# Optimization experiments

Hardware: AMD Instinct MI355X
Metric: run time of the kernel (lower is better)

Reference implementation:

```python
import jax, jax.numpy as jnp
import numpy as np

NUM_HIGH = 3
CHANNELS = 3

def _gauss_kernel(channels):
    k = jnp.array([[1., 4., 6., 4., 1.],
                   [4., 16., 24., 16., 4.],
                   [6., 24., 36., 24., 6.],
                   [4., 16., 24., 16., 4.],
                   [1., 4., 6., 4., 1.]], dtype=jnp.float32) / 256.0
    # depthwise kernel layout OIHW with I=1, O=channels
    return jnp.broadcast_to(k, (channels, 1, 5, 5))

def conv_gauss(img, kernel):
    # reflect-pad by 2 on H,W then depthwise (grouped) 5x5 conv, VALID
    p = jnp.pad(img, ((0, 0), (0, 0), (2, 2), (2, 2)), mode='reflect')
    return jax.lax.conv_general_dilated(
        p, kernel, window_strides=(1, 1), padding='VALID',
        feature_group_count=img.shape[1],
        dimension_numbers=('NCHW', 'OIHW', 'NCHW'))

def downsample(x):
    return x[:, :, ::2, ::2]

def upsample(x, kernel):
    B, C, H, W = x.shape
    x_up = jnp.zeros((B, C, 2 * H, 2 * W), dtype=x.dtype).at[:, :, ::2, ::2].set(x)
    return conv_gauss(x_up, 4.0 * kernel)

def setup_inputs() -> dict:
    key = jax.random.key(0)
    img = jax.random.normal(key, (8, CHANNELS, 1024, 1024), dtype=jnp.float32)
    kernel = _gauss_kernel(CHANNELS)
    return {"img": img, "kernel": kernel}

def reference(img, kernel):
    # pyramid_decom: Laplacian pyramid (H,W divisible by 2**NUM_HIGH, so no interpolate)
    current = img
    pyr = []
    for _ in range(NUM_HIGH):
        filtered = conv_gauss(current, kernel)
        down = downsample(filtered)
        up = upsample(down, kernel)
        pyr.append(current - up)
        current = down
    pyr.append(current)
    return tuple(pyr)
```

## Files before the change

### kernel.cpp

```cpp
#include <hip/hip_runtime.h>

#define TW 64
#define TH 32
#define DR 18
#define DC 34
#define TMPP 76
#define SDP 35

__device__ __forceinline__ int refl(int t, int n) {
    if (t < 0) t = -t;
    if (t >= n) t = 2 * (n - 1) - t;
    return t;
}

__global__ __launch_bounds__(256, 8) void lap_level_kernel(
    const float* __restrict__ cur, float* __restrict__ lap,
    float* __restrict__ down, int H, int W)
{
    __shared__ float s_tmp[DR][TMPP];
    __shared__ float s_down[DR][SDP];

    const int x0 = blockIdx.x * TW, y0 = blockIdx.y * TH;
    const int img = blockIdx.z;
    const int Hh = H >> 1, Wh = W >> 1;
    const int tid = threadIdx.x;

    const float* curb = cur + (size_t)img * H * W;

    const bool border = (x0 == 0) | (y0 == 0) | (x0 + TW == W) | (y0 + TH == H);
    if (!border) {
        for (int k = tid; k < DR * 18; k += 256) {
            unsigned a = (unsigned)k / 18u;
            unsigned c4 = ((unsigned)k - a * 18u) * 4u;
            const float* p = curb + (size_t)(y0 + 2 * (int)a - 4) * W + (x0 - 4 + (int)c4);
            float4 r0 = *(const float4*)(p);
            float4 r1 = *(const float4*)(p + (size_t)W);
            float4 r2 = *(const float4*)(p + (size_t)2 * W);
            float4 r3 = *(const float4*)(p + (size_t)3 * W);
            float4 r4 = *(const float4*)(p + (size_t)4 * W);
            float4 t;
            t.x = r0.x + 4.f * r1.x + 6.f * r2.x + 4.f * r3.x + r4.x;
            t.y = r0.y + 4.f * r1.y + 6.f * r2.y + 4.f * r3.y + r4.y;
            t.z = r0.z + 4.f * r1.z + 6.f * r2.z + 4.f * r3.z + r4.z;
            t.w = r0.w + 4.f * r1.w + 6.f * r2.w + 4.f * r3.w + r4.w;
            *(float4*)&s_tmp[a][c4] = t;
        }
    } else {
        for (int k = tid; k < DR * 72; k += 256) {
            unsigned a = (unsigned)k / 72u;
            unsigned c = (unsigned)k - a * 72u;
            int gx = refl(x0 - 4 + (int)c, W);
            int r0 = y0 + 2 * (int)a - 4;
            float acc = 0.f;
            const float wv[5] = {1.f, 4.f, 6.f, 4.f, 1.f};
#pragma unroll
            for (int u = 0; u < 5; ++u)
                acc += wv[u] * curb[(size_t)refl(r0 + u, H) * W + gx];
            s_tmp[a][c] = acc;
        }
    }
    __syncthreads();

    float* downb = down + (size_t)img * Hh * Wh;
    for (int k = tid; k < DR * 17; k += 256) {
        unsigned a = (unsigned)k / 17u;
        unsigned b2 = (unsigned)k - a * 17u;
        float4 A = *(const float4*)&s_tmp[a][4 * b2];
        float4 B = *(const float4*)&s_tmp[a][4 * b2 + 4];
        float v0 = (A.x + 4.f * A.y + 6.f * A.z + 4.f * A.w + B.x) * (1.f / 256.f);
        float v1 = (A.z + 4.f * A.w + 6.f * B.x + 4.f * B.y + B.z) * (1.f / 256.f);
        s_down[a][2 * b2] = v0;
        s_down[a][2 * b2 + 1] = v1;
        if (a - 1u < 16u) {
            size_t rowoff = (size_t)((y0 >> 1) - 1 + (int)a) * Wh + ((x0 >> 1) - 1);
            if (b2 >= 1u) downb[rowoff + 2 * b2] = v0;
            if (b2 <= 15u) downb[rowoff + 2 * b2 + 1] = v1;
        }
    }
    __syncthreads();

    const int tx = tid & 15, ty = tid >> 4;
    float d0[4], d1[4], d2[4];
#pragma unroll
    for (int c = 0; c < 4; ++c) {
        d0[c] = s_down[ty + 0][2 * tx + c];
        d1[c] = s_down[ty + 1][2 * tx + c];
        d2[c] = s_down[ty + 2][2 * tx + c];
    }
    float ce[4], co[4];
#pragma unroll
    for (int c = 0; c < 4; ++c) {
        ce[c] = d0[c] + 6.f * d1[c] + d2[c];
        co[c] = 4.f * (d1[c] + d2[c]);
    }
    const int i0 = y0 + 2 * ty, j0 = x0 + 4 * tx;
    const float* cvp = curb + (size_t)i0 * W + j0;
    float4 cve = *(const float4*)(cvp);
    float4 cvo = *(const float4*)(cvp + (size_t)W);
    float4 oe, oo;
    oe.x = cve.x - (ce[0] + 6.f * ce[1] + ce[2]) * (1.f / 64.f);
    oe.y = cve.y - 4.f * (ce[1] + ce[2]) * (1.f / 64.f);
    oe.z = cve.z - (ce[1] + 6.f * ce[2] + ce[3]) * (1.f / 64.f);
    oe.w = cve.w - 4.f * (ce[2] + ce[3]) * (1.f / 64.f);
    oo.x = cvo.x - (co[0] + 6.f * co[1] + co[2]) * (1.f / 64.f);
    oo.y = cvo.y - 4.f * (co[1] + co[2]) * (1.f / 64.f);
    oo.z = cvo.z - (co[1] + 6.f * co[2] + co[3]) * (1.f / 64.f);
    oo.w = cvo.w - 4.f * (co[2] + co[3]) * (1.f / 64.f);

    float* lapb = lap + (size_t)img * H * W;
    *(float4*)(lapb + (size_t)i0 * W + j0) = oe;
    *(float4*)(lapb + (size_t)(i0 + 1) * W + j0) = oo;
}

extern "C" void kernel_launch(void* const* d_in, const int* in_sizes, int n_in,
                              void* d_out, int out_size, void* d_ws, size_t ws_size,
                              hipStream_t stream) {
    const float* img = (const float*)d_in[0];
    float* out = (float*)d_out;

    const long long BC = 8LL * 3;
    const long long n0 = BC * 1024 * 1024;
    const long long n1 = BC * 512 * 512;
    const long long n2 = BC * 256 * 256;

    float* out0 = out;
    float* out1 = out0 + n0;
    float* out2 = out1 + n1;
    float* out3 = out2 + n2;

    float* ws0 = (float*)d_ws;
    float* ws1 = ws0 + n1;

    lap_level_kernel<<<dim3(1024 / TW, 1024 / TH, (int)BC), 256, 0, stream>>>(
        img, out0, ws0, 1024, 1024);
    lap_level_kernel<<<dim3(512 / TW, 512 / TH, (int)BC), 256, 0, stream>>>(
        ws0, out1, ws1, 512, 512);
    lap_level_kernel<<<dim3(256 / TW, 256 / TH, (int)BC), 256, 0, stream>>>(
        ws1, out2, out3, 256, 256);
}
```

Before: 81.03 us.

## Fuse vertical and horizontal blur into one pass, drop intermediate smem stage

Merges the vertical 5-tap pass and the horizontal 5-tap/downsample pass into a single per-thread computation that reads two float4s per row directly from global memory. This removes the s_tmp shared buffer and one __syncthreads. The center-pixel loads are hoisted to the top of the kernel so their latency overlaps the blur work, and the Laplacian output uses nontemporal stores. In exchange, the overlapping 8-wide reads fetch more global data, roughly twice the column loads, which the cache must absorb.

```diff
diff --git a/kernel.cpp b/kernel.cpp
--- a/kernel.cpp
+++ b/kernel.cpp
@@ -4,8 +4,10 @@
 #define TH 32
 #define DR 18
 #define DC 34
-#define TMPP 76
 #define SDP 35
+#define NTASK (DR * 17)
+
+typedef float vf4 __attribute__((ext_vector_type(4)));
 
 __device__ __forceinline__ int refl(int t, int n) {
     if (t < 0) t = -t;
@@ -13,73 +15,92 @@
     return t;
 }
 
+__device__ __forceinline__ void nt_store4(float x, float y, float z, float w, float* p) {
+    vf4 v = {x, y, z, w};
+    __builtin_nontemporal_store(v, (vf4*)p);
+}
+
 __global__ __launch_bounds__(256, 8) void lap_level_kernel(
     const float* __restrict__ cur, float* __restrict__ lap,
     float* __restrict__ down, int H, int W)
 {
-    __shared__ float s_tmp[DR][TMPP];
     __shared__ float s_down[DR][SDP];
 
     const int x0 = blockIdx.x * TW, y0 = blockIdx.y * TH;
     const int img = blockIdx.z;
     const int Hh = H >> 1, Wh = W >> 1;
     const int tid = threadIdx.x;
+    const int tx = tid & 15, ty = tid >> 4;
 
     const float* curb = cur + (size_t)img * H * W;
 
+    const int i0 = y0 + 2 * ty, j0 = x0 + 4 * tx;
+    const float* cvp = curb + (size_t)i0 * W + j0;
+    const float4 cve = *(const float4*)(cvp);
+    const float4 cvo = *(const float4*)(cvp + (size_t)W);
+
+    float* downb = down + (size_t)img * Hh * Wh;
     const bool border = (x0 == 0) | (y0 == 0) | (x0 + TW == W) | (y0 + TH == H);
     if (!border) {
-        for (int k = tid; k < DR * 18; k += 256) {
-            unsigned a = (unsigned)k / 18u;
-            unsigned c4 = ((unsigned)k - a * 18u) * 4u;
-            const float* p = curb + (size_t)(y0 + 2 * (int)a - 4) * W + (x0 - 4 + (int)c4);
-            float4 r0 = *(const float4*)(p);
-            float4 r1 = *(const float4*)(p + (size_t)W);
-            float4 r2 = *(const float4*)(p + (size_t)2 * W);
-            float4 r3 = *(const float4*)(p + (size_t)3 * W);
-            float4 r4 = *(const float4*)(p + (size_t)4 * W);
-            float4 t;
-            t.x = r0.x + 4.f * r1.x + 6.f * r2.x + 4.f * r3.x + r4.x;
-            t.y = r0.y + 4.f * r1.y + 6.f * r2.y + 4.f * r3.y + r4.y;
-            t.z = r0.z + 4.f * r1.z + 6.f * r2.z + 4.f * r3.z + r4.z;
-            t.w = r0.w + 4.f * r1.w + 6.f * r2.w + 4.f * r3.w + r4.w;
-            *(float4*)&s_tmp[a][c4] = t;
+        for (int k = tid; k < NTASK; k += 256) {
+            unsigned a = (unsigned)k / 17u;
+            unsigned b2 = (unsigned)k - a * 17u;
+            const float* p = curb + (size_t)(y0 - 4 + 2 * (int)a) * W + (x0 - 4 + 4 * (int)b2);
+            float4 A0 = *(const float4*)(p);
+            float4 B0 = *(const float4*)(p + 4);
+            float4 A1 = *(const float4*)(p + (size_t)W);
+            float4 B1 = *(const float4*)(p + (size_t)W + 4);
+            float4 A2 = *(const float4*)(p + (size_t)2 * W);
+            float4 B2 = *(const float4*)(p + (size_t)2 * W + 4);
+            float4 A3 = *(const float4*)(p + (size_t)3 * W);
+            float4 B3 = *(const float4*)(p + (size_t)3 * W + 4);
+            float4 A4 = *(const float4*)(p + (size_t)4 * W);
+            float4 B4 = *(const float4*)(p + (size_t)4 * W + 4);
+            float s0 = A0.x + 4.f * A1.x + 6.f * A2.x + 4.f * A3.x + A4.x;
+            float s1 = A0.y + 4.f * A1.y + 6.f * A2.y + 4.f * A3.y + A4.y;
+            float s2 = A0.z + 4.f * A1.z + 6.f * A2.z + 4.f * A3.z + A4.z;
+            float s3 = A0.w + 4.f * A1.w + 6.f * A2.w + 4.f * A3.w + A4.w;
+            float s4 = B0.x + 4.f * B1.x + 6.f * B2.x + 4.f * B3.x + B4.x;
+            float s5 = B0.y + 4.f * B1.y + 6.f * B2.y + 4.f * B3.y + B4.y;
+            float s6 = B0.z + 4.f * B1.z + 6.f * B2.z + 4.f * B3.z + B4.z;
+            float v0 = (s0 + 4.f * s1 + 6.f * s2 + 4.f * s3 + s4) * (1.f / 256.f);
+            float v1 = (s2 + 4.f * s3 + 6.f * s4 + 4.f * s5 + s6) * (1.f / 256.f);
+            s_down[a][2 * b2] = v0;
+            s_down[a][2 * b2 + 1] = v1;
+            if (a - 1u < 16u) {
+                size_t rowoff = (size_t)((y0 >> 1) - 1 + (int)a) * Wh + ((x0 >> 1) - 1);
+                if (b2 >= 1u) downb[rowoff + 2 * b2] = v0;
+                if (b2 <= 15u) downb[rowoff + 2 * b2 + 1] = v1;
+            }
         }
     } else {
-        for (int k = tid; k < DR * 72; k += 256) {
-            unsigned a = (unsigned)k / 72u;
-            unsigned c = (unsigned)k - a * 72u;
-            int gx = refl(x0 - 4 + (int)c, W);
-            int r0 = y0 + 2 * (int)a - 4;
-            float acc = 0.f;
+        for (int k = tid; k < NTASK; k += 256) {
+            unsigned a = (unsigned)k / 17u;
+            unsigned b2 = (unsigned)k - a * 17u;
             const float wv[5] = {1.f, 4.f, 6.f, 4.f, 1.f};
+            float s[7];
 #pragma unroll
-            for (int u = 0; u < 5; ++u)
-                acc += wv[u] * curb[(size_t)refl(r0 + u, H) * W + gx];
-            s_tmp[a][c] = acc;
+            for (int c = 0; c < 7; ++c) {
+                int gx = refl(x0 - 4 + 4 * (int)b2 + c, W);
+                float acc = 0.f;
+#pragma unroll
+                for (int u = 0; u < 5; ++u)
+                    acc += wv[u] * curb[(size_t)refl(y0 - 4 + 2 * (int)a + u, H) * W + gx];
+                s[c] = acc;
+            }
+            float v0 = (s[0] + 4.f * s[1] + 6.f * s[2] + 4.f * s[3] + s[4]) * (1.f / 256.f);
+            float v1 = (s[2] + 4.f * s[3] + 6.f * s[4] + 4.f * s[5] + s[6]) * (1.f / 256.f);
+            s_down[a][2 * b2] = v0;
+            s_down[a][2 * b2 + 1] = v1;
+            if (a - 1u < 16u) {
+                size_t rowoff = (size_t)((y0 >> 1) - 1 + (int)a) * Wh + ((x0 >> 1) - 1);
+                if (b2 >= 1u) downb[rowoff + 2 * b2] = v0;
+                if (b2 <= 15u) downb[rowoff + 2 * b2 + 1] = v1;
+            }
         }
     }
     __syncthreads();
 
-    float* downb = down + (size_t)img * Hh * Wh;
-    for (int k = tid; k < DR * 17; k += 256) {
-        unsigned a = (unsigned)k / 17u;
-        unsigned b2 = (unsigned)k - a * 17u;
-        float4 A = *(const float4*)&s_tmp[a][4 * b2];
-        float4 B = *(const float4*)&s_tmp[a][4 * b2 + 4];
-        float v0 = (A.x + 4.f * A.y + 6.f * A.z + 4.f * A.w + B.x) * (1.f / 256.f);
-        float v1 = (A.z + 4.f * A.w + 6.f * B.x + 4.f * B.y + B.z) * (1.f / 256.f);
-        s_down[a][2 * b2] = v0;
-        s_down[a][2 * b2 + 1] = v1;
-        if (a - 1u < 16u) {
-            size_t rowoff = (size_t)((y0 >> 1) - 1 + (int)a) * Wh + ((x0 >> 1) - 1);
-            if (b2 >= 1u) downb[rowoff + 2 * b2] = v0;
-            if (b2 <= 15u) downb[rowoff + 2 * b2 + 1] = v1;
-        }
-    }
-    __syncthreads();
-
-    const int tx = tid & 15, ty = tid >> 4;
     float d0[4], d1[4], d2[4];
 #pragma unroll
     for (int c = 0; c < 4; ++c) {
@@ -93,23 +114,17 @@
         ce[c] = d0[c] + 6.f * d1[c] + d2[c];
         co[c] = 4.f * (d1[c] + d2[c]);
     }
-    const int i0 = y0 + 2 * ty, j0 = x0 + 4 * tx;
-    const float* cvp = curb + (size_t)i0 * W + j0;
-    float4 cve = *(const float4*)(cvp);
-    float4 cvo = *(const float4*)(cvp + (size_t)W);
-    float4 oe, oo;
-    oe.x = cve.x - (ce[0] + 6.f * ce[1] + ce[2]) * (1.f / 64.f);
-    oe.y = cve.y - 4.f * (ce[1] + ce[2]) * (1.f / 64.f);
-    oe.z = cve.z - (ce[1] + 6.f * ce[2] + ce[3]) * (1.f / 64.f);
-    oe.w = cve.w - 4.f * (ce[2] + ce[3]) * (1.f / 64.f);
-    oo.x = cvo.x - (co[0] + 6.f * co[1] + co[2]) * (1.f / 64.f);
-    oo.y = cvo.y - 4.f * (co[1] + co[2]) * (1.f / 64.f);
-    oo.z = cvo.z - (co[1] + 6.f * co[2] + co[3]) * (1.f / 64.f);
-    oo.w = cvo.w - 4.f * (co[2] + co[3]) * (1.f / 64.f);
-
     float* lapb = lap + (size_t)img * H * W;
-    *(float4*)(lapb + (size_t)i0 * W + j0) = oe;
-    *(float4*)(lapb + (size_t)(i0 + 1) * W + j0) = oo;
+    nt_store4(cve.x - (ce[0] + 6.f * ce[1] + ce[2]) * (1.f / 64.f),
+              cve.y - 4.f * (ce[1] + ce[2]) * (1.f / 64.f),
+              cve.z - (ce[1] + 6.f * ce[2] + ce[3]) * (1.f / 64.f),
+              cve.w - 4.f * (ce[2] + ce[3]) * (1.f / 64.f),
+              lapb + (size_t)i0 * W + j0);
+    nt_store4(cvo.x - (co[0] + 6.f * co[1] + co[2]) * (1.f / 64.f),
+              cvo.y - 4.f * (co[1] + co[2]) * (1.f / 64.f),
+              cvo.z - (co[1] + 6.f * co[2] + co[3]) * (1.f / 64.f),
+              cvo.w - 4.f * (co[2] + co[3]) * (1.f / 64.f),
+              lapb + (size_t)(i0 + 1) * W + j0);
 }
 
 extern "C" void kernel_launch(void* const* d_in, const int* in_sizes, int n_in,
```

New measurement: 185.2 us. 2.29x slower.

## Widen tiles to 128 columns and compute two filtered rows per thread

Applied to the files above, without the earlier changes.

Doubles the tile width to 128 columns, so each thread in the final stage produces 8 Laplacian outputs per row instead of 4, and the column halo overhead per tile shrinks. The vertical filter pass now has each thread load 7 input rows and emit two downsampled-row partial sums, reusing 3 rows between them. The separate border and interior paths are merged into one path that reflects row indices always and falls back to scalar gathers only for edge columns. Fewer blocks and more work per thread trade parallelism for reuse, and at the smaller levels the grid becomes small, with fewer blocks to spread across the CUs.

```diff
diff --git a/kernel.cpp b/kernel.cpp
--- a/kernel.cpp
+++ b/kernel.cpp
@@ -1,11 +1,11 @@
 #include <hip/hip_runtime.h>
 
-#define TW 64
+#define TW 128
 #define TH 32
 #define DR 18
-#define DC 34
-#define TMPP 76
-#define SDP 35
+#define NC4 34
+#define TMPP 140
+#define SDP 67
 
 __device__ __forceinline__ int refl(int t, int n) {
     if (t < 0) t = -t;
@@ -27,89 +27,102 @@
 
     const float* curb = cur + (size_t)img * H * W;
 
-    const bool border = (x0 == 0) | (y0 == 0) | (x0 + TW == W) | (y0 + TH == H);
-    if (!border) {
-        for (int k = tid; k < DR * 18; k += 256) {
-            unsigned a = (unsigned)k / 18u;
-            unsigned c4 = ((unsigned)k - a * 18u) * 4u;
-            const float* p = curb + (size_t)(y0 + 2 * (int)a - 4) * W + (x0 - 4 + (int)c4);
-            float4 r0 = *(const float4*)(p);
-            float4 r1 = *(const float4*)(p + (size_t)W);
-            float4 r2 = *(const float4*)(p + (size_t)2 * W);
-            float4 r3 = *(const float4*)(p + (size_t)3 * W);
-            float4 r4 = *(const float4*)(p + (size_t)4 * W);
-            float4 t;
-            t.x = r0.x + 4.f * r1.x + 6.f * r2.x + 4.f * r3.x + r4.x;
-            t.y = r0.y + 4.f * r1.y + 6.f * r2.y + 4.f * r3.y + r4.y;
-            t.z = r0.z + 4.f * r1.z + 6.f * r2.z + 4.f * r3.z + r4.z;
-            t.w = r0.w + 4.f * r1.w + 6.f * r2.w + 4.f * r3.w + r4.w;
-            *(float4*)&s_tmp[a][c4] = t;
+    for (int k = tid; k < 9 * NC4; k += 256) {
+        int e = k / NC4, c4 = k - e * NC4;
+        int colg = x0 - 4 + 4 * c4;
+        int rows[7];
+#pragma unroll
+        for (int u = 0; u < 7; ++u) rows[u] = refl(y0 - 4 + 4 * e + u, H);
+        float4 r[7];
+        if (colg >= 0 && colg + 3 < W) {
+#pragma unroll
+            for (int u = 0; u < 7; ++u)
+                r[u] = *(const float4*)(curb + (size_t)rows[u] * W + colg);
+        } else {
+            int gx[4];
+#pragma unroll
+            for (int cc = 0; cc < 4; ++cc) gx[cc] = refl(colg + cc, W);
+#pragma unroll
+            for (int u = 0; u < 7; ++u) {
+                const float* rp = curb + (size_t)rows[u] * W;
+                r[u].x = rp[gx[0]]; r[u].y = rp[gx[1]];
+                r[u].z = rp[gx[2]]; r[u].w = rp[gx[3]];
+            }
         }
-    } else {
-        for (int k = tid; k < DR * 72; k += 256) {
-            unsigned a = (unsigned)k / 72u;
-            unsigned c = (unsigned)k - a * 72u;
-            int gx = refl(x0 - 4 + (int)c, W);
-            int r0 = y0 + 2 * (int)a - 4;
-            float acc = 0.f;
-            const float wv[5] = {1.f, 4.f, 6.f, 4.f, 1.f};
-#pragma unroll
-            for (int u = 0; u < 5; ++u)
-                acc += wv[u] * curb[(size_t)refl(r0 + u, H) * W + gx];
-            s_tmp[a][c] = acc;
-        }
+        float4 t0, t1;
+        t0.x = r[0].x + 4.f * r[1].x + 6.f * r[2].x + 4.f * r[3].x + r[4].x;
+        t0.y = r[0].y + 4.f * r[1].y + 6.f * r[2].y + 4.f * r[3].y + r[4].y;
+        t0.z = r[0].z + 4.f * r[1].z + 6.f * r[2].z + 4.f * r[3].z + r[4].z;
+        t0.w = r[0].w + 4.f * r[1].w + 6.f * r[2].w + 4.f * r[3].w + r[4].w;
+        t1.x = r[2].x + 4.f * r[3].x + 6.f * r[4].x + 4.f * r[5].x + r[6].x;
+        t1.y = r[2].y + 4.f * r[3].y + 6.f * r[4].y + 4.f * r[5].y + r[6].y;
+        t1.z = r[2].z + 4.f * r[3].z + 6.f * r[4].z + 4.f * r[5].z + r[6].z;
+        t1.w = r[2].w + 4.f * r[3].w + 6.f * r[4].w + 4.f * r[5].w + r[6].w;
+        *(float4*)&s_tmp[2 * e][4 * c4] = t0;
+        *(float4*)&s_tmp[2 * e + 1][4 * c4] = t1;
     }
     __syncthreads();
 
     float* downb = down + (size_t)img * Hh * Wh;
-    for (int k = tid; k < DR * 17; k += 256) {
-        unsigned a = (unsigned)k / 17u;
-        unsigned b2 = (unsigned)k - a * 17u;
+    for (int k = tid; k < DR * 33; k += 256) {
+        int a = k / 33, b2 = k - a * 33;
         float4 A = *(const float4*)&s_tmp[a][4 * b2];
         float4 B = *(const float4*)&s_tmp[a][4 * b2 + 4];
         float v0 = (A.x + 4.f * A.y + 6.f * A.z + 4.f * A.w + B.x) * (1.f / 256.f);
         float v1 = (A.z + 4.f * A.w + 6.f * B.x + 4.f * B.y + B.z) * (1.f / 256.f);
         s_down[a][2 * b2] = v0;
         s_down[a][2 * b2 + 1] = v1;
-        if (a - 1u < 16u) {
-            size_t rowoff = (size_t)((y0 >> 1) - 1 + (int)a) * Wh + ((x0 >> 1) - 1);
-            if (b2 >= 1u) downb[rowoff + 2 * b2] = v0;
-            if (b2 <= 15u) downb[rowoff + 2 * b2 + 1] = v1;
+        if ((unsigned)(a - 1) < 16u) {
+            size_t rowoff = (size_t)((y0 >> 1) - 1 + a) * Wh + ((x0 >> 1) - 1);
+            if (b2 >= 1) downb[rowoff + 2 * b2] = v0;
+            if (b2 <= 31) downb[rowoff + 2 * b2 + 1] = v1;
         }
     }
     __syncthreads();
 
     const int tx = tid & 15, ty = tid >> 4;
-    float d0[4], d1[4], d2[4];
+    float d0[6], d1[6], d2[6];
 #pragma unroll
-    for (int c = 0; c < 4; ++c) {
-        d0[c] = s_down[ty + 0][2 * tx + c];
-        d1[c] = s_down[ty + 1][2 * tx + c];
-        d2[c] = s_down[ty + 2][2 * tx + c];
+    for (int c = 0; c < 6; ++c) {
+        d0[c] = s_down[ty + 0][4 * tx + c];
+        d1[c] = s_down[ty + 1][4 * tx + c];
+        d2[c] = s_down[ty + 2][4 * tx + c];
     }
-    float ce[4], co[4];
+    float ce[6], co[6];
 #pragma unroll
-    for (int c = 0; c < 4; ++c) {
+    for (int c = 0; c < 6; ++c) {
         ce[c] = d0[c] + 6.f * d1[c] + d2[c];
         co[c] = 4.f * (d1[c] + d2[c]);
     }
-    const int i0 = y0 + 2 * ty, j0 = x0 + 4 * tx;
+    const int i0 = y0 + 2 * ty, j0 = x0 + 8 * tx;
     const float* cvp = curb + (size_t)i0 * W + j0;
-    float4 cve = *(const float4*)(cvp);
-    float4 cvo = *(const float4*)(cvp + (size_t)W);
-    float4 oe, oo;
-    oe.x = cve.x - (ce[0] + 6.f * ce[1] + ce[2]) * (1.f / 64.f);
-    oe.y = cve.y - 4.f * (ce[1] + ce[2]) * (1.f / 64.f);
-    oe.z = cve.z - (ce[1] + 6.f * ce[2] + ce[3]) * (1.f / 64.f);
-    oe.w = cve.w - 4.f * (ce[2] + ce[3]) * (1.f / 64.f);
-    oo.x = cvo.x - (co[0] + 6.f * co[1] + co[2]) * (1.f / 64.f);
-    oo.y = cvo.y - 4.f * (co[1] + co[2]) * (1.f / 64.f);
-    oo.z = cvo.z - (co[1] + 6.f * co[2] + co[3]) * (1.f / 64.f);
-    oo.w = cvo.w - 4.f * (co[2] + co[3]) * (1.f / 64.f);
+    float4 ce0 = *(const float4*)(cvp);
+    float4 ce1 = *(const float4*)(cvp + 4);
+    float4 co0 = *(const float4*)(cvp + (size_t)W);
+    float4 co1 = *(const float4*)(cvp + (size_t)W + 4);
+    float4 oe0, oe1, oo0, oo1;
+    oe0.x = ce0.x - (ce[0] + 6.f * ce[1] + ce[2]) * (1.f / 64.f);
+    oe0.y = ce0.y - 4.f * (ce[1] + ce[2]) * (1.f / 64.f);
+    oe0.z = ce0.z - (ce[1] + 6.f * ce[2] + ce[3]) * (1.f / 64.f);
+    oe0.w = ce0.w - 4.f * (ce[2] + ce[3]) * (1.f / 64.f);
+    oe1.x = ce1.x - (ce[2] + 6.f * ce[3] + ce[4]) * (1.f / 64.f);
+    oe1.y = ce1.y - 4.f * (ce[3] + ce[4]) * (1.f / 64.f);
+    oe1.z = ce1.z - (ce[3] + 6.f * ce[4] + ce[5]) * (1.f / 64.f);
+    oe1.w = ce1.w - 4.f * (ce[4] + ce[5]) * (1.f / 64.f);
+    oo0.x = co0.x - (co[0] + 6.f * co[1] + co[2]) * (1.f / 64.f);
+    oo0.y = co0.y - 4.f * (co[1] + co[2]) * (1.f / 64.f);
+    oo0.z = co0.z - (co[1] + 6.f * co[2] + co[3]) * (1.f / 64.f);
+    oo0.w = co0.w - 4.f * (co[2] + co[3]) * (1.f / 64.f);
+    oo1.x = co1.x - (co[2] + 6.f * co[3] + co[4]) * (1.f / 64.f);
+    oo1.y = co1.y - 4.f * (co[3] + co[4]) * (1.f / 64.f);
+    oo1.z = co1.z - (co[3] + 6.f * co[4] + co[5]) * (1.f / 64.f);
+    oo1.w = co1.w - 4.f * (co[4] + co[5]) * (1.f / 64.f);
 
     float* lapb = lap + (size_t)img * H * W;
-    *(float4*)(lapb + (size_t)i0 * W + j0) = oe;
-    *(float4*)(lapb + (size_t)(i0 + 1) * W + j0) = oo;
+    *(float4*)(lapb + (size_t)i0 * W + j0) = oe0;
+    *(float4*)(lapb + (size_t)i0 * W + j0 + 4) = oe1;
+    *(float4*)(lapb + (size_t)(i0 + 1) * W + j0) = oo0;
+    *(float4*)(lapb + (size_t)(i0 + 1) * W + j0 + 4) = oo1;
 }
 
 extern "C" void kernel_launch(void* const* d_in, const int* in_sizes, int n_in,
```

After: 111.5 us. +37.6%, slower.
